# Kernel tuning notes

Hardware: AMD Instinct MI355X
Metric: run time of the kernel (lower is better)

## Reference

```python
import jax, jax.numpy as jnp
import numpy as np

N_NODES = 50000
IN_CH = 128
HID = 128
N_EDGES = 800000


def _glorot(key, shape):
    fan_in, fan_out = shape[0], shape[1]
    lim = (6.0 / (fan_in + fan_out)) ** 0.5
    return jax.random.uniform(key, shape, jnp.float32, -lim, lim)


def setup_inputs() -> dict:
    key = jax.random.key(0)
    ks = jax.random.split(key, 8)
    x = jax.random.normal(ks[0], (N_NODES, IN_CH), jnp.float32)
    edge_index = jax.random.randint(ks[1], (2, N_EDGES), 0, N_NODES, jnp.int64)
    return {
        "x": x,
        "edge_index": edge_index,
        # SAGEConv1: lin_l (with bias) applied to mean-aggregated neighbors,
        # lin_r (no bias) applied to root features (PyG defaults, mean aggr)
        "W1l": _glorot(ks[2], (IN_CH, HID)),
        "b1l": jnp.zeros((HID,), jnp.float32),
        "W1r": _glorot(ks[3], (IN_CH, HID)),
        # SAGEConv2
        "W2l": _glorot(ks[4], (HID, HID)),
        "b2l": jnp.zeros((HID,), jnp.float32),
        "W2r": _glorot(ks[5], (HID, HID)),
        # final Linear(hidden, 1)
        "Wout": _glorot(ks[6], (HID, 1)),
        "bout": jnp.zeros((1,), jnp.float32),
    }


def _sage_conv(x, src, dst, Wl, bl, Wr, n_nodes):
    # gather source features along edges, mean-reduce into destinations
    msgs = x[src]                                                # [E, D]
    sums = jax.ops.segment_sum(msgs, dst, num_segments=n_nodes)  # [N, D]
    cnt = jax.ops.segment_sum(jnp.ones((src.shape[0], 1), x.dtype), dst,
                              num_segments=n_nodes)              # [N, 1]
    agg = sums / jnp.maximum(cnt, 1.0)
    return agg @ Wl + bl + x @ Wr


def reference(x, edge_index, W1l, b1l, W1r, W2l, b2l, W2r, Wout, bout):
    src, dst = edge_index[0], edge_index[1]
    n = x.shape[0]
    h = jax.nn.relu(_sage_conv(x, src, dst, W1l, b1l, W1r, n))
    h = jax.nn.relu(_sage_conv(h, src, dst, W2l, b2l, W2r, n))
    return (h @ Wout + bout).squeeze(-1)  # [N]
```

## Files before the change

kernel.cpp:

```cpp
#include <hip/hip_runtime.h>

#define D 128
#define LSTR 132
#define CAP 3072
#define NBLK 256

typedef __attribute__((ext_vector_type(8))) short short8;
typedef __attribute__((ext_vector_type(4))) float f32x4;

static __device__ __forceinline__ unsigned short f2bf(float f) {
    unsigned u = __float_as_uint(f);
    return (unsigned short)((u + 0x7fffu + ((u >> 16) & 1u)) >> 16);
}
static __device__ __forceinline__ float b2f(unsigned short u) {
    return __uint_as_float(((unsigned)u) << 16);
}


__global__ __launch_bounds__(256) void prep_hist_kernel(
    const float* __restrict__ x, const float* __restrict__ W1l,
    const float* __restrict__ W1r, const float* __restrict__ W2l,
    const float* __restrict__ W2r, unsigned* __restrict__ xb2,
    unsigned short* __restrict__ Bt1, unsigned short* __restrict__ Bt2,
    int NX2, const int* __restrict__ dst, int E, int nbins,
    unsigned* __restrict__ G, int* __restrict__ gctr) {
    const int t = threadIdx.x;
    if (blockIdx.x < NBLK) {
        __shared__ int h[2048];
        for (int i = t; i < nbins; i += 256) h[i] = 0;
        __syncthreads();
        const int per = (E + NBLK - 1) / NBLK;
        const int lo = blockIdx.x * per;
        const int hi = min(lo + per, E);
        for (int i = lo + t; i < hi; i += 256) atomicAdd(&h[dst[i] >> 5], 1);
        __syncthreads();
        for (int i = t; i < nbins; i += 256)
            G[(size_t)i * NBLK + blockIdx.x] = (unsigned)h[i];
        return;
    }
    if (blockIdx.x == NBLK && t == 0) *gctr = 0;
    const int i = (blockIdx.x - NBLK) * 256 + t;
    if (i < NX2) {
        const float2 v = *(const float2*)(x + 2 * (size_t)i);
        xb2[i] = (unsigned)f2bf(v.x) | ((unsigned)f2bf(v.y) << 16);
    } else if (i < NX2 + 2 * 32768) {
        const int j = i - NX2;
        const int which = j >> 15;
        const int jj = j & 32767;
        const int n = jj >> 8;
        const int k = jj & 255;
        const float* Wl = which ? W2l : W1l;
        const float* Wr = which ? W2r : W1r;
        const float w = (k < 128) ? Wl[k * 128 + n] : Wr[(k - 128) * 128 + n];
        (which ? Bt2 : Bt1)[jj] = f2bf(w);
    }
}

__global__ __launch_bounds__(256) void scanB_kernel(unsigned* __restrict__ G,
                                                    int nbins,
                                                    int* __restrict__ tile_base,
                                                    int* __restrict__ gctr) {
    const int wave = threadIdx.x >> 6;
    const int lane = threadIdx.x & 63;
    const int bin = blockIdx.x * 4 + wave;
    if (bin >= nbins) return;
    unsigned* p = G + (size_t)bin * NBLK + lane * 4;
    uint4 v = *(uint4*)p;
    const unsigned s = v.x + v.y + v.z + v.w;
    unsigned sc = s;
#pragma unroll
    for (int off = 1; off < 64; off <<= 1) {
        const unsigned u = (unsigned)__shfl_up((int)sc, off, 64);
        if (lane >= off) sc += u;
    }
    const unsigned excl = sc - s;
    uint4 w;
    w.x = excl;
    w.y = excl + v.x;
    w.z = excl + v.x + v.y;
    w.w = excl + v.x + v.y + v.z;
    *(uint4*)p = w;
    const unsigned tot = __shfl((int)(excl + s), 63, 64);
    int base = 0;
    if (lane == 63) base = atomicAdd(gctr, (int)tot);
    base = __shfl(base, 63, 64);
    if (lane == 0) {
        tile_base[2 * bin] = base;
        tile_base[2 * bin + 1] = base + (int)tot;
    }
}

__global__ __launch_bounds__(256) void fillB_kernel(
    const int* __restrict__ src, const int* __restrict__ dst, int E,
    const unsigned* __restrict__ G, const int* __restrict__ tile_base,
    unsigned* __restrict__ csr, int nbins) {
    __shared__ int rank[2048];
    __shared__ int base[2048];
    const int t = threadIdx.x;
    for (int i = t; i < nbins; i += 256) {
        rank[i] = 0;
        base[i] = tile_base[2 * i] + (int)G[(size_t)i * NBLK + blockIdx.x];
    }
    __syncthreads();
    const int per = (E + NBLK - 1) / NBLK;
    const int lo = blockIdx.x * per;
    const int hi = min(lo + per, E);
    for (int i = lo + t; i < hi; i += 256) {
        const int d = dst[i];
        const int bin = d >> 5;
        const int r = atomicAdd(&rank[bin], 1);
        csr[base[bin] + r] = (unsigned)src[i] | ((unsigned)d << 16);
    }
}

__global__ __launch_bounds__(256) void sortT_kernel(unsigned* __restrict__ csr,
                                                    const int* __restrict__
                                                        tile_base,
                                                    float* __restrict__ invL_g,
                                                    int N) {
    __shared__ unsigned sortedE[CAP];
    __shared__ int rowcnt[32];
    __shared__ int rowofs[32];
    const int b = blockIdx.x;
    const int i0 = b * 32;
    const int t = threadIdx.x;
    const int rs0 = tile_base[2 * b];
    const int re0 = tile_base[2 * b + 1];
    const int nE = re0 - rs0;

    if (t < 32) rowcnt[t] = 0;
    __syncthreads();
    for (int i = t; i < nE; i += 256)
        atomicAdd(&rowcnt[(csr[rs0 + i] >> 16) & 31], 1);
    __syncthreads();
    if (t < 32) {
        const int v = rowcnt[t];
        if (i0 + t < N) invL_g[i0 + t] = 1.0f / fmaxf((float)v, 1.0f);
        int s = v;
#pragma unroll
        for (int off = 1; off < 32; off <<= 1) {
            const int u = __shfl_up(s, off, 32);
            if ((t & 31) >= off) s += u;
        }
        rowofs[t] = s - v;
    }
    __syncthreads();
    if (nE <= CAP) {
        for (int i = t; i < nE; i += 256) {
            const unsigned p = csr[rs0 + i];
            const int k = atomicAdd(&rowofs[(p >> 16) & 31], 1);
            sortedE[k] = p;
        }
        __syncthreads();
        for (int i = t; i < nE; i += 256) csr[rs0 + i] = sortedE[i];
    }
}

template <bool HEAD>
__global__ __launch_bounds__(256) void sage_kernel(
    const unsigned short* __restrict__ xb, const unsigned* __restrict__ csr,
    const int* __restrict__ tile_base, const float* __restrict__ invL_g,
    const unsigned short* __restrict__ Bt,
    const float* __restrict__ bl, const float* __restrict__ Wout,
    const float* __restrict__ bout, unsigned short* __restrict__ hb_out,
    float* __restrict__ out, int N) {
    __shared__ float aggL[32 * LSTR];
    __shared__ float invL[32];
    __shared__ float redH[64];

    const int b = blockIdx.x;
    const int i0 = b * 32;
    const int t = threadIdx.x;
    const int g = t >> 5;
    const int l = t & 31;
    const int c4 = l << 2;

    for (int i = t; i < 32 * LSTR; i += 256) aggL[i] = 0.f;
    if (t < 32) invL[t] = (i0 + t < N) ? invL_g[i0 + t] : 1.0f;
    __syncthreads();

    const int rs0 = tile_base[2 * b];
    const int re0 = tile_base[2 * b + 1];
    const int nE = re0 - rs0;
    int e = rs0 + ((nE * g) >> 3);
    const int ee = rs0 + ((nE * (g + 1)) >> 3);

    float4 acc = make_float4(0.f, 0.f, 0.f, 0.f);
    int cur = (e < ee) ? (int)(csr[e] >> 16) - i0 : -1;

    auto load4 = [&](unsigned p) -> float4 {
        const ushort4 u =
            *(const ushort4*)(xb + (size_t)(p & 0xffffu) * D + c4);
        float4 v;
        v.x = b2f(u.x); v.y = b2f(u.y); v.z = b2f(u.z); v.w = b2f(u.w);
        return v;
    };
    auto step = [&](unsigned p, const float4& v) {
        const int r = (int)(p >> 16) - i0;
        if (r != cur) {
            float* q = aggL + cur * LSTR + c4;
            atomicAdd(q + 0, acc.x);
            atomicAdd(q + 1, acc.y);
            atomicAdd(q + 2, acc.z);
            atomicAdd(q + 3, acc.w);
            acc = make_float4(0.f, 0.f, 0.f, 0.f);
            cur = r;
        }
        acc.x += v.x; acc.y += v.y; acc.z += v.z; acc.w += v.w;
    };

    while (e + 16 <= ee) {
        unsigned p[16];
        float4 v[16];
#pragma unroll
        for (int j = 0; j < 16; ++j) p[j] = csr[e + j];
#pragma unroll
        for (int j = 0; j < 16; ++j) v[j] = load4(p[j]);
#pragma unroll
        for (int j = 0; j < 16; ++j) step(p[j], v[j]);
        e += 16;
    }
    if (e + 8 <= ee) {
        unsigned p[8];
        float4 v[8];
#pragma unroll
        for (int j = 0; j < 8; ++j) p[j] = csr[e + j];
#pragma unroll
        for (int j = 0; j < 8; ++j) v[j] = load4(p[j]);
#pragma unroll
        for (int j = 0; j < 8; ++j) step(p[j], v[j]);
        e += 8;
    }
    while (e < ee) {
        const unsigned p = csr[e];
        step(p, load4(p));
        ++e;
    }
    if (cur >= 0) {
        float* q = aggL + cur * LSTR + c4;
        atomicAdd(q + 0, acc.x);
        atomicAdd(q + 1, acc.y);
        atomicAdd(q + 2, acc.z);
        atomicAdd(q + 3, acc.w);
    }
    __syncthreads();

    const int wave = t >> 6;
    const int lane = t & 63;
    const int ln = lane & 15;
    const int quad = lane >> 4;
    const int mtile = wave & 1;
    const int nt0 = (wave >> 1) * 4;
    const int mrow = mtile * 16 + ln;
    const int gmr = i0 + mrow;
    const float inv = invL[mrow];

    f32x4 acc4[4] = {f32x4{0.f, 0.f, 0.f, 0.f}, f32x4{0.f, 0.f, 0.f, 0.f},
                     f32x4{0.f, 0.f, 0.f, 0.f}, f32x4{0.f, 0.f, 0.f, 0.f}};

#pragma unroll
    for (int s = 0; s < 4; ++s) {
        const int kb = s * 32 + quad * 8;
        const float* ap = aggL + mrow * LSTR + kb;
        const float4 fa = *(const float4*)ap;
        const float4 fb = *(const float4*)(ap + 4);
        const short8 aA = {(short)f2bf(fa.x * inv), (short)f2bf(fa.y * inv),
                           (short)f2bf(fa.z * inv), (short)f2bf(fa.w * inv),
                           (short)f2bf(fb.x * inv), (short)f2bf(fb.y * inv),
                           (short)f2bf(fb.z * inv), (short)f2bf(fb.w * inv)};
        short8 aX = {0, 0, 0, 0, 0, 0, 0, 0};
        if (gmr < N) aX = *(const short8*)(xb + (size_t)gmr * D + kb);
#pragma unroll
        for (int nt = 0; nt < 4; ++nt) {
            const int n = (nt0 + nt) * 16 + ln;
            const short8 b1 = *(const short8*)(Bt + n * 256 + kb);
            const short8 b2 = *(const short8*)(Bt + n * 256 + 128 + kb);
            acc4[nt] = __builtin_amdgcn_mfma_f32_16x16x32_bf16(aA, b1, acc4[nt],
                                                               0, 0, 0);
            acc4[nt] = __builtin_amdgcn_mfma_f32_16x16x32_bf16(aX, b2, acc4[nt],
                                                               0, 0, 0);
        }
    }

    float biasv[4], woutv[4];
#pragma unroll
    for (int nt = 0; nt < 4; ++nt) {
        const int col = (nt0 + nt) * 16 + ln;
        biasv[nt] = bl[col];
        if (HEAD) woutv[nt] = Wout[col];
    }

    if (!HEAD) {
#pragma unroll
        for (int r = 0; r < 4; ++r) {
            const int gr = i0 + mtile * 16 + quad * 4 + r;
            if (gr < N) {
#pragma unroll
                for (int nt = 0; nt < 4; ++nt) {
                    const int col = (nt0 + nt) * 16 + ln;
                    const float v = fmaxf(acc4[nt][r] + biasv[nt], 0.f);
                    hb_out[(size_t)gr * D + col] = f2bf(v);
                }
            }
        }
    } else {
        const float b0 = bout[0];
#pragma unroll
        for (int r = 0; r < 4; ++r) {
            const int row = mtile * 16 + quad * 4 + r;
            float p = 0.f;
#pragma unroll
            for (int nt = 0; nt < 4; ++nt) {
                const float v = fmaxf(acc4[nt][r] + biasv[nt], 0.f);
                p += v * woutv[nt];
            }
            p += __shfl_xor(p, 1);
            p += __shfl_xor(p, 2);
            p += __shfl_xor(p, 4);
            p += __shfl_xor(p, 8);
            if (ln == 0) redH[row * 2 + (wave >> 1)] = p;
        }
        __syncthreads();
        if (t < 32) {
            const int gr = i0 + t;
            if (gr < N) out[gr] = redH[t * 2] + redH[t * 2 + 1] + b0;
        }
    }
}

extern "C" void kernel_launch(void* const* d_in, const int* in_sizes, int n_in,
                              void* d_out, int out_size, void* d_ws,
                              size_t ws_size, hipStream_t stream) {
    const float* x = (const float*)d_in[0];
    const int* ei = (const int*)d_in[1];
    const float* W1l = (const float*)d_in[2];
    const float* b1l = (const float*)d_in[3];
    const float* W1r = (const float*)d_in[4];
    const float* W2l = (const float*)d_in[5];
    const float* b2l = (const float*)d_in[6];
    const float* W2r = (const float*)d_in[7];
    const float* Wout = (const float*)d_in[8];
    const float* bout = (const float*)d_in[9];

    const int N = in_sizes[0] / D;
    const int E = in_sizes[1] / 2;
    const int* src = ei;
    const int* dst = ei + E;

    const int nbins = (N + 31) / 32;
    const size_t Npad = (size_t)((N + 255) & ~255);
    const size_t Epad = (size_t)((E + 255) & ~255);

    int* tile_base = (int*)d_ws;
    int* gctr = tile_base + 4096;
    float* invL_g = (float*)(gctr + 4);
    unsigned* G = (unsigned*)(invL_g + Npad);
    unsigned* csr = G + (size_t)2048 * NBLK;
    unsigned short* xb = (unsigned short*)(csr + Epad);
    unsigned short* hb = xb + (size_t)N * D;
    unsigned short* Bt1 = hb + (size_t)N * D;
    unsigned short* Bt2 = Bt1 + 128 * 256;
    float* out = (float*)d_out;

    const int NX2 = N * D / 2;
    const int prep_blocks = (NX2 + 2 * 32768 + 255) / 256;

    prep_hist_kernel<<<NBLK + prep_blocks, 256, 0, stream>>>(
        x, W1l, W1r, W2l, W2r, (unsigned*)xb, Bt1, Bt2, NX2, dst, E, nbins, G,
        gctr);
    scanB_kernel<<<(nbins + 3) / 4, 256, 0, stream>>>(G, nbins, tile_base,
                                                      gctr);
    fillB_kernel<<<NBLK, 256, 0, stream>>>(src, dst, E, G, tile_base, csr,
                                           nbins);
    sortT_kernel<<<nbins, 256, 0, stream>>>(csr, tile_base, invL_g, N);

    sage_kernel<false><<<nbins, 256, 0, stream>>>(
        xb, csr, tile_base, invL_g, Bt1, b1l, nullptr, nullptr, hb, nullptr, N);
    sage_kernel<true><<<nbins, 256, 0, stream>>>(
        hb, csr, tile_base, invL_g, Bt2, b2l, Wout, bout, nullptr, out, N);
}
```

Before: 277.3 us.

## Split fused SAGE kernel into two-half aggregation and separate GEMM kernels

Splits the fused gather-aggregate-plus-MFMA kernel into an aggregation kernel, launched with twice as many blocks where each block handles half of a tile's edges, and a GEMM kernel that sums the two bf16 partial aggregates before the matmul. The intent is more parallelism and better latency hiding in the memory-bound gather phase. In exchange it writes and re-reads two N×128 bf16 partial buffers per layer, adds extra launches, and rounds the partial sums to bf16 before they are combined. It also reduces the gather unroll from 16 to 8.

```diff
diff --git a/kernel.cpp b/kernel.cpp
--- a/kernel.cpp
+++ b/kernel.cpp
@@ -156,19 +156,14 @@
     }
 }
 
-template <bool HEAD>
-__global__ __launch_bounds__(256) void sage_kernel(
+__global__ __launch_bounds__(256) void agg_kernel(
     const unsigned short* __restrict__ xb, const unsigned* __restrict__ csr,
-    const int* __restrict__ tile_base, const float* __restrict__ invL_g,
-    const unsigned short* __restrict__ Bt,
-    const float* __restrict__ bl, const float* __restrict__ Wout,
-    const float* __restrict__ bout, unsigned short* __restrict__ hb_out,
-    float* __restrict__ out, int N) {
+    const int* __restrict__ tile_base, unsigned short* __restrict__ P, int N) {
     __shared__ float aggL[32 * LSTR];
-    __shared__ float invL[32];
-    __shared__ float redH[64];
-
-    const int b = blockIdx.x;
+
+    const int bx = blockIdx.x;
+    const int b = bx >> 1;
+    const int half = bx & 1;
     const int i0 = b * 32;
     const int t = threadIdx.x;
     const int g = t >> 5;
@@ -176,14 +171,14 @@
     const int c4 = l << 2;
 
     for (int i = t; i < 32 * LSTR; i += 256) aggL[i] = 0.f;
-    if (t < 32) invL[t] = (i0 + t < N) ? invL_g[i0 + t] : 1.0f;
     __syncthreads();
 
     const int rs0 = tile_base[2 * b];
     const int re0 = tile_base[2 * b + 1];
     const int nE = re0 - rs0;
-    int e = rs0 + ((nE * g) >> 3);
-    const int ee = rs0 + ((nE * (g + 1)) >> 3);
+    const int seg = half * 8 + g;
+    int e = rs0 + ((nE * seg) >> 4);
+    const int ee = rs0 + ((nE * (seg + 1)) >> 4);
 
     float4 acc = make_float4(0.f, 0.f, 0.f, 0.f);
     int cur = (e < ee) ? (int)(csr[e] >> 16) - i0 : -1;
@@ -209,26 +204,16 @@
         acc.x += v.x; acc.y += v.y; acc.z += v.z; acc.w += v.w;
     };
 
-    while (e + 16 <= ee) {
-        unsigned p[16];
-        float4 v[16];
-#pragma unroll
-        for (int j = 0; j < 16; ++j) p[j] = csr[e + j];
-#pragma unroll
-        for (int j = 0; j < 16; ++j) v[j] = load4(p[j]);
-#pragma unroll
-        for (int j = 0; j < 16; ++j) step(p[j], v[j]);
-        e += 16;
-    }
-    if (e + 8 <= ee) {
-        unsigned p[8];
-        float4 v[8];
-#pragma unroll
-        for (int j = 0; j < 8; ++j) p[j] = csr[e + j];
-#pragma unroll
-        for (int j = 0; j < 8; ++j) v[j] = load4(p[j]);
-#pragma unroll
-        for (int j = 0; j < 8; ++j) step(p[j], v[j]);
+    while (e + 8 <= ee) {
+        const unsigned p0 = csr[e + 0], p1 = csr[e + 1];
+        const unsigned p2 = csr[e + 2], p3 = csr[e + 3];
+        const unsigned p4 = csr[e + 4], p5 = csr[e + 5];
+        const unsigned p6 = csr[e + 6], p7 = csr[e + 7];
+        const float4 v0 = load4(p0), v1 = load4(p1), v2 = load4(p2),
+                     v3 = load4(p3), v4 = load4(p4), v5 = load4(p5),
+                     v6 = load4(p6), v7 = load4(p7);
+        step(p0, v0); step(p1, v1); step(p2, v2); step(p3, v3);
+        step(p4, v4); step(p5, v5); step(p6, v6); step(p7, v7);
         e += 8;
     }
     while (e < ee) {
@@ -245,6 +230,35 @@
     }
     __syncthreads();
 
+    const int row = t >> 3;
+    const int ch0 = (t & 7) * 16;
+    const int gr = i0 + row;
+    if (gr < N) {
+        const float* ap = aggL + row * LSTR + ch0;
+        short8 o1, o2;
+#pragma unroll
+        for (int j = 0; j < 8; ++j) o1[j] = (short)f2bf(ap[j]);
+#pragma unroll
+        for (int j = 0; j < 8; ++j) o2[j] = (short)f2bf(ap[8 + j]);
+        unsigned short* q = P + ((size_t)half * N + gr) * D + ch0;
+        *(short8*)q = o1;
+        *(short8*)(q + 8) = o2;
+    }
+}
+
+template <bool HEAD>
+__global__ __launch_bounds__(256) void gemm_kernel(
+    const unsigned short* __restrict__ xb, const unsigned short* __restrict__ P,
+    const float* __restrict__ invL_g,
+    const unsigned short* __restrict__ Bt,
+    const float* __restrict__ bl, const float* __restrict__ Wout,
+    const float* __restrict__ bout, unsigned short* __restrict__ hb_out,
+    float* __restrict__ out, int N) {
+    __shared__ float redH[64];
+
+    const int b = blockIdx.x;
+    const int i0 = b * 32;
+    const int t = threadIdx.x;
     const int wave = t >> 6;
     const int lane = t & 63;
     const int ln = lane & 15;
@@ -253,7 +267,11 @@
     const int nt0 = (wave >> 1) * 4;
     const int mrow = mtile * 16 + ln;
     const int gmr = i0 + mrow;
-    const float inv = invL[mrow];
+    const bool valid = gmr < N;
+    const float inv = valid ? invL_g[gmr] : 0.f;
+    const unsigned short* p1 = P + (size_t)gmr * D;
+    const unsigned short* p2 = P + ((size_t)N + gmr) * D;
+    const unsigned short* px = xb + (size_t)gmr * D;
 
     f32x4 acc4[4] = {f32x4{0.f, 0.f, 0.f, 0.f}, f32x4{0.f, 0.f, 0.f, 0.f},
                      f32x4{0.f, 0.f, 0.f, 0.f}, f32x4{0.f, 0.f, 0.f, 0.f}};
@@ -261,15 +279,19 @@
 #pragma unroll
     for (int s = 0; s < 4; ++s) {
         const int kb = s * 32 + quad * 8;
-        const float* ap = aggL + mrow * LSTR + kb;
-        const float4 fa = *(const float4*)ap;
-        const float4 fb = *(const float4*)(ap + 4);
-        const short8 aA = {(short)f2bf(fa.x * inv), (short)f2bf(fa.y * inv),
-                           (short)f2bf(fa.z * inv), (short)f2bf(fa.w * inv),
-                           (short)f2bf(fb.x * inv), (short)f2bf(fb.y * inv),
-                           (short)f2bf(fb.z * inv), (short)f2bf(fb.w * inv)};
+        short8 aA = {0, 0, 0, 0, 0, 0, 0, 0};
         short8 aX = {0, 0, 0, 0, 0, 0, 0, 0};
-        if (gmr < N) aX = *(const short8*)(xb + (size_t)gmr * D + kb);
+        if (valid) {
+            const short8 u1 = *(const short8*)(p1 + kb);
+            const short8 u2 = *(const short8*)(p2 + kb);
+#pragma unroll
+            for (int j = 0; j < 8; ++j) {
+                const float a = b2f((unsigned short)u1[j]) +
+                                b2f((unsigned short)u2[j]);
+                aA[j] = (short)f2bf(a * inv);
+            }
+            aX = *(const short8*)(px + kb);
+        }
 #pragma unroll
         for (int nt = 0; nt < 4; ++nt) {
             const int n = (nt0 + nt) * 16 + ln;
@@ -360,6 +382,7 @@
     unsigned short* hb = xb + (size_t)N * D;
     unsigned short* Bt1 = hb + (size_t)N * D;
     unsigned short* Bt2 = Bt1 + 128 * 256;
+    unsigned short* P = Bt2 + 128 * 256;
     float* out = (float*)d_out;
 
     const int NX2 = N * D / 2;
@@ -374,8 +397,10 @@
                                            nbins);
     sortT_kernel<<<nbins, 256, 0, stream>>>(csr, tile_base, invL_g, N);
 
-    sage_kernel<false><<<nbins, 256, 0, stream>>>(
-        xb, csr, tile_base, invL_g, Bt1, b1l, nullptr, nullptr, hb, nullptr, N);
-    sage_kernel<true><<<nbins, 256, 0, stream>>>(
-        hb, csr, tile_base, invL_g, Bt2, b2l, Wout, bout, nullptr, out, N);
-}
+    agg_kernel<<<2 * nbins, 256, 0, stream>>>(xb, csr, tile_base, P, N);
+    gemm_kernel<false><<<nbins, 256, 0, stream>>>(
+        xb, P, invL_g, Bt1, b1l, nullptr, nullptr, hb, nullptr, N);
+    agg_kernel<<<2 * nbins, 256, 0, stream>>>(hb, csr, tile_base, P, N);
+    gemm_kernel<true><<<nbins, 256, 0, stream>>>(
+        hb, P, invL_g, Bt2, b2l, Wout, bout, nullptr, out, N);
+}
```

After: 327.5 us. 18.1% more time.
